# Kernel tuning notes

Hardware: AMD Instinct MI355X
Metric: run time of the kernel (lower is better)

## Reference

```python
import jax, jax.numpy as jnp
import numpy as np

N_NODES = 70839  # num_user + num_item from config
N_EDGES = 2_000_000
EMB_DIM = 64
EPS = 1e-12  # torch F.normalize default eps


def setup_inputs() -> dict:
    key = jax.random.key(0)
    k1, k2, k3, k4 = jax.random.split(key, 4)
    ego_embedding = jax.random.normal(k1, (N_NODES, EMB_DIM), dtype=jnp.float32)
    edge_weight = jax.random.uniform(k2, (N_EDGES,), dtype=jnp.float32)
    edge_src = jax.random.randint(k3, (N_EDGES,), 0, N_NODES, dtype=jnp.int32)
    edge_dst = jax.random.randint(k4, (N_EDGES,), 0, N_NODES, dtype=jnp.int32)
    return {
        "ego_embedding": ego_embedding,
        "edge_weight": edge_weight,
        "edge_src": edge_src,
        "edge_dst": edge_dst,
    }


def reference(ego_embedding, edge_weight, edge_src, edge_dst):
    # message: m_e = h[src_e] * w_e   (u_mul_e)
    m = ego_embedding[edge_src] * edge_weight[:, None]          # [E, D]
    # reduce: h_v = sum_{e: dst_e = v} m_e   (fn.sum)
    h = jax.ops.segment_sum(m, edge_dst, num_segments=N_NODES)  # [N, D]
    # F.normalize(h, dim=1, p=2): x / max(||x||_2, eps)
    norm = jnp.linalg.norm(h, axis=1, keepdims=True)
    return h / jnp.maximum(norm, EPS)
```

## Files before the change

kernel.cpp:

```cpp
#include <hip/hip_runtime.h>
#include <hip/hip_fp16.h>

#define EMB_D 64
#define SB 1024
#define SPAN 128
#define MAXG 1024
#define MAXK 3072
#define NCHUNK2 512
#define CHMAX 4096
#define TILE 4096
#define SLICE_SH 14
#define CAST_BLOCKS 256


__device__ __forceinline__ float h15_to_float(unsigned int bits) {
    return __half2float(__ushort_as_half((unsigned short)bits));
}

__global__ void a1_cast_histK(const float2* __restrict__ embin,
                              __half2* __restrict__ emb16, int n2,
                              const int* __restrict__ src,
                              const int* __restrict__ dst,
                              int* __restrict__ cntT,
                              int E, int NK, int S, int chunk) {
    if (blockIdx.x < CAST_BLOCKS) {
        int i = blockIdx.x * blockDim.x + threadIdx.x;
        int st = CAST_BLOCKS * blockDim.x;
        for (; i < n2; i += st)
            emb16[i] = __float22half2_rn(embin[i]);
    } else {
        __shared__ int bins[MAXK];
        int hb = blockIdx.x - CAST_BLOCKS;
        for (int k = threadIdx.x; k < NK; k += blockDim.x) bins[k] = 0;
        __syncthreads();
        int beg = hb * chunk;
        int end = min(beg + chunk, E);
        for (int i = beg + threadIdx.x; i < end; i += blockDim.x) {
            int key = (dst[i] >> 7) * S + (src[i] >> SLICE_SH);
            atomicAdd(&bins[key], 1);
        }
        __syncthreads();
        for (int k = threadIdx.x; k < NK; k += blockDim.x)
            cntT[k * NCHUNK2 + hb] = bins[k];
    }
}

__global__ void a1_cast_hist(const float2* __restrict__ embin,
                             __half2* __restrict__ emb16, int n2,
                             const int* __restrict__ dst,
                             int* __restrict__ cntT,
                             int E, int G, int chunk) {
    if (blockIdx.x < CAST_BLOCKS) {
        int i = blockIdx.x * blockDim.x + threadIdx.x;
        int st = CAST_BLOCKS * blockDim.x;
        for (; i < n2; i += st)
            emb16[i] = __float22half2_rn(embin[i]);
    } else {
        __shared__ int bins[MAXG];
        int hb = blockIdx.x - CAST_BLOCKS;
        for (int g = threadIdx.x; g < G; g += blockDim.x) bins[g] = 0;
        __syncthreads();
        int beg = hb * chunk;
        int end = min(beg + chunk, E);
        for (int i = beg + threadIdx.x; i < end; i += blockDim.x)
            atomicAdd(&bins[dst[i] >> 7], 1);
        __syncthreads();
        for (int g = threadIdx.x; g < G; g += blockDim.x)
            cntT[g * NCHUNK2 + hb] = bins[g];
    }
}

__global__ void scan_reduceB(const int* __restrict__ counts,
                             int* __restrict__ partial, int M) {
    __shared__ int wsum[16];
    const int tid = threadIdx.x, lane = tid & 63, wid = tid >> 6;
    int i = blockIdx.x * SB + tid;
    int v = (i < M) ? counts[i] : 0;
    #pragma unroll
    for (int off = 32; off > 0; off >>= 1)
        v += __shfl_xor(v, off, 64);
    if (lane == 0) wsum[wid] = v;
    __syncthreads();
    if (tid == 0) {
        int s = 0;
        #pragma unroll
        for (int k = 0; k < 16; ++k) s += wsum[k];
        partial[blockIdx.x] = s;
    }
}

__global__ void scan_partials(const int* __restrict__ partial,
                              int* __restrict__ blockoff,
                              int* __restrict__ offsets, int numB, int M) {
    __shared__ int wsum[16];
    __shared__ int wpre[16];
    __shared__ int carry;
    const int tid = threadIdx.x, lane = tid & 63, wid = tid >> 6;
    if (tid == 0) carry = 0;
    const int nPass = (numB + SB - 1) / SB;
    for (int p = 0; p < nPass; ++p) {
        __syncthreads();
        int base = carry;
        int idx = p * SB + tid;
        int v = (idx < numB) ? partial[idx] : 0;
        int x = v;
        #pragma unroll
        for (int off = 1; off < 64; off <<= 1) {
            int t = __shfl_up(x, off, 64);
            if (lane >= off) x += t;
        }
        if (lane == 63) wsum[wid] = x;
        __syncthreads();
        if (wid == 0) {
            int s = (lane < 16) ? wsum[lane] : 0;
            #pragma unroll
            for (int off = 1; off < 16; off <<= 1) {
                int t = __shfl_up(s, off, 64);
                if (lane >= off) s += t;
            }
            if (lane < 16) wpre[lane] = s;
        }
        __syncthreads();
        int excl = base + ((wid > 0) ? wpre[wid - 1] : 0) + (x - v);
        if (idx < numB) blockoff[idx] = excl;
        __syncthreads();
        if (tid == 0) carry = base + wpre[15];
    }
    __syncthreads();
    if (tid == 0) offsets[M] = carry;
}

__global__ void scan_applyB(const int* __restrict__ counts,
                            const int* __restrict__ blockoff,
                            int* __restrict__ offsets, int M) {
    __shared__ int wsum[16];
    __shared__ int wpre[16];
    const int tid = threadIdx.x, lane = tid & 63, wid = tid >> 6;
    int i = blockIdx.x * SB + tid;
    int v = (i < M) ? counts[i] : 0;
    int x = v;
    #pragma unroll
    for (int off = 1; off < 64; off <<= 1) {
        int t = __shfl_up(x, off, 64);
        if (lane >= off) x += t;
    }
    if (lane == 63) wsum[wid] = x;
    __syncthreads();
    if (wid == 0) {
        int s = (lane < 16) ? wsum[lane] : 0;
        #pragma unroll
        for (int off = 1; off < 16; off <<= 1) {
            int t = __shfl_up(s, off, 64);
            if (lane >= off) s += t;
        }
        if (lane < 16) wpre[lane] = s;
    }
    __syncthreads();
    int excl = blockoff[blockIdx.x] + ((wid > 0) ? wpre[wid - 1] : 0) + (x - v);
    if (i < M) offsets[i] = excl;
}

__global__ void scan_apply_ip(int* __restrict__ data,
                              const int* __restrict__ blockoff, int M) {
    __shared__ int wsum[16];
    __shared__ int wpre[16];
    const int tid = threadIdx.x, lane = tid & 63, wid = tid >> 6;
    int i = blockIdx.x * SB + tid;
    int v = (i < M) ? data[i] : 0;
    int x = v;
    #pragma unroll
    for (int off = 1; off < 64; off <<= 1) {
        int t = __shfl_up(x, off, 64);
        if (lane >= off) x += t;
    }
    if (lane == 63) wsum[wid] = x;
    __syncthreads();
    if (wid == 0) {
        int s = (lane < 16) ? wsum[lane] : 0;
        #pragma unroll
        for (int off = 1; off < 16; off <<= 1) {
            int t = __shfl_up(s, off, 64);
            if (lane >= off) s += t;
        }
        if (lane < 16) wpre[lane] = s;
    }
    __syncthreads();
    int excl = blockoff[blockIdx.x] + ((wid > 0) ? wpre[wid - 1] : 0) + (x - v);
    if (i < M) data[i] = excl;
}

__global__ __launch_bounds__(512) void partition_sortK(
        const int* __restrict__ src,
        const int* __restrict__ dst,
        const float* __restrict__ w,
        const int* __restrict__ scanT,
        uint2* __restrict__ stream8,
        int E, int NK, int S, int chunk) {
    __shared__ uint2 recs[CHMAX];
    __shared__ int cur[MAXK];
    __shared__ int delta[MAXK];
    __shared__ int wtot[8];

    const int tid = threadIdx.x, lane = tid & 63, wv = tid >> 6;
    const int b = blockIdx.x;
    const int beg = b * chunk;
    const int end = min(beg + chunk, E);
    const int n = end - beg;

    const int K = (NK + 511) >> 9;
    int vals[6], bases[6];
    int acc = 0;
    #pragma unroll
    for (int k = 0; k < 6; ++k) {
        int key = tid * K + k;
        int c = 0, bs = 0;
        if (k < K && key < NK) {
            bs = scanT[key * NCHUNK2 + b];
            c = scanT[key * NCHUNK2 + b + 1] - bs;
        }
        vals[k] = c;
        bases[k] = bs;
        acc += c;
    }
    int x = acc;
    #pragma unroll
    for (int off = 1; off < 64; off <<= 1) {
        int t = __shfl_up(x, off, 64);
        if (lane >= off) x += t;
    }
    if (lane == 63) wtot[wv] = x;
    __syncthreads();
    int woff = 0;
    #pragma unroll
    for (int k2 = 0; k2 < 8; ++k2)
        woff += (k2 < wv) ? wtot[k2] : 0;
    int run = woff + x - acc;
    #pragma unroll
    for (int k = 0; k < 6; ++k) {
        int key = tid * K + k;
        if (k < K && key < NK) {
            cur[key] = run;
            delta[key] = bases[k] - run;
            run += vals[k];
        }
    }
    __syncthreads();

    for (int i = beg + tid; i < end; i += 512) {
        int d = dst[i];
        int key = (d >> 7) * S + (src[i] >> SLICE_SH);
        unsigned int wb = __half_as_ushort(__float2half_rn(w[i]));
        unsigned int pk = ((unsigned int)src[i] << 15) | (wb & 0x7FFFu);
        int j = atomicAdd(&cur[key], 1);
        recs[j] = make_uint2(pk, (unsigned int)(d & (SPAN - 1)) |
                                 ((unsigned int)key << 7));
    }
    __syncthreads();

    for (int j = tid; j < n; j += 512) {
        uint2 r = recs[j];
        int key = (int)(r.y >> 7);
        stream8[delta[key] + j] = make_uint2(r.x, r.y & (SPAN - 1u));
    }
}

__global__ __launch_bounds__(512) void partition_sort(
        const int* __restrict__ src,
        const int* __restrict__ dst,
        const float* __restrict__ w,
        const int* __restrict__ cntT,
        const int* __restrict__ scanT,
        uint2* __restrict__ stream8,
        int E, int G, int chunk) {
    __shared__ uint2 recs[CHMAX];
    __shared__ int cur[MAXG];
    __shared__ int delta[MAXG];
    __shared__ int wtot[8];

    const int tid = threadIdx.x, lane = tid & 63, wv = tid >> 6;
    const int b = blockIdx.x;
    const int beg = b * chunk;
    const int end = min(beg + chunk, E);
    const int n = end - beg;

    const int K = (G + 511) >> 9;
    int vals[2];
    int acc = 0;
    #pragma unroll
    for (int k = 0; k < 2; ++k) {
        int g = tid * K + k;
        int c = (k < K && g < G) ? cntT[g * NCHUNK2 + b] : 0;
        vals[k] = c;
        acc += c;
    }
    int x = acc;
    #pragma unroll
    for (int off = 1; off < 64; off <<= 1) {
        int t = __shfl_up(x, off, 64);
        if (lane >= off) x += t;
    }
    if (lane == 63) wtot[wv] = x;
    __syncthreads();
    int woff = 0;
    #pragma unroll
    for (int k2 = 0; k2 < 8; ++k2)
        woff += (k2 < wv) ? wtot[k2] : 0;
    int run = woff + x - acc;
    #pragma unroll
    for (int k = 0; k < 2; ++k) {
        int g = tid * K + k;
        if (k < K && g < G) {
            cur[g] = run;
            delta[g] = scanT[g * NCHUNK2 + b] - run;
            run += vals[k];
        }
    }
    __syncthreads();

    for (int i = beg + tid; i < end; i += 512) {
        int d = dst[i];
        unsigned int wb = __half_as_ushort(__float2half_rn(w[i]));
        unsigned int pk = ((unsigned int)src[i] << 15) | (wb & 0x7FFFu);
        int g = d >> 7;
        int j = atomicAdd(&cur[g], 1);
        recs[j] = make_uint2(pk, (unsigned int)(d & (SPAN - 1)) |
                                 ((unsigned int)g << 7));
    }
    __syncthreads();

    for (int j = tid; j < n; j += 512) {
        uint2 r = recs[j];
        int g = (int)(r.y >> 7);
        stream8[delta[g] + j] = make_uint2(r.x, r.y & (SPAN - 1u));
    }
}

__global__ __launch_bounds__(512) void gather_fused(
        const char* __restrict__ emb16b,
        const uint2* __restrict__ stream8,
        const int* __restrict__ scanT,
        float* __restrict__ out, int N, int SN) {
    __shared__ uint2 lrec[TILE];
    __shared__ unsigned int srt[TILE];
    __shared__ int hcnt[SPAN];
    __shared__ int nstart[SPAN];
    __shared__ int cur[SPAN];
    __shared__ int wtot[2];

    const int g = blockIdx.x;
    const int tid = threadIdx.x;
    const int lane = tid & 63, wv = tid >> 6;
    const int base = scanT[(size_t)g * SN];
    const int endE = scanT[(size_t)(g + 1) * SN];
    const int crew = tid >> 4;
    const int ql = tid & 15;
    const int sub = ql >> 3;
    const int sl = ql & 7;
    const unsigned qlo = (unsigned)(sl << 4);

    float4 accA[4], accB[4];
    #pragma unroll
    for (int ni = 0; ni < 4; ++ni) {
        accA[ni] = make_float4(0.f, 0.f, 0.f, 0.f);
        accB[ni] = make_float4(0.f, 0.f, 0.f, 0.f);
    }

    for (int tb = base; tb < endE; tb += TILE) {
        const int n = min(TILE, endE - tb);
        if (tid < SPAN) hcnt[tid] = 0;
        __syncthreads();
        for (int j = tid; j < n; j += 512) {
            uint2 r = stream8[tb + j];
            lrec[j] = r;
            atomicAdd(&hcnt[r.y], 1);
        }
        __syncthreads();
        int v = (tid < SPAN) ? hcnt[tid] : 0;
        int x = v;
        #pragma unroll
        for (int off = 1; off < 64; off <<= 1) {
            int t = __shfl_up(x, off, 64);
            if (lane >= off) x += t;
        }
        if (wv < 2 && lane == 63) wtot[wv] = x;
        __syncthreads();
        if (tid < SPAN) {
            int excl = x - v + ((wv == 1) ? wtot[0] : 0);
            nstart[tid] = excl;
            cur[tid] = excl;
        }
        __syncthreads();
        for (int j = tid; j < n; j += 512) {
            uint2 r = lrec[j];
            int slot = atomicAdd(&cur[r.y], 1);
            srt[slot] = r.x;
        }
        __syncthreads();
        #pragma unroll
        for (int ni = 0; ni < 4; ++ni) {
            int nd = crew + (ni << 5);
            int s = nstart[nd];
            int e = cur[nd];
            float4 aA = accA[ni];
            float4 aB = accB[ni];
            int k0 = s + sub;
            unsigned int pk0 = (k0 < e) ? srt[k0] : 0u;
            uint4 r0 = *reinterpret_cast<const uint4*>(
                emb16b + ((pk0 >> 15) * 128u + qlo));
            for (int k = k0; k < e; k += 2) {
                int k1 = k + 2;
                unsigned int pk1 = (k1 < e) ? srt[k1] : 0u;
                uint4 r1 = *reinterpret_cast<const uint4*>(
                    emb16b + ((pk1 >> 15) * 128u + qlo));
                float wt = h15_to_float(pk0 & 0x7FFFu);
                float2 x01 = __half22float2(*reinterpret_cast<__half2*>(&r0.x));
                float2 x23 = __half22float2(*reinterpret_cast<__half2*>(&r0.y));
                float2 x45 = __half22float2(*reinterpret_cast<__half2*>(&r0.z));
                float2 x67 = __half22float2(*reinterpret_cast<__half2*>(&r0.w));
                aA.x = fmaf(x01.x, wt, aA.x);
                aA.y = fmaf(x01.y, wt, aA.y);
                aA.z = fmaf(x23.x, wt, aA.z);
                aA.w = fmaf(x23.y, wt, aA.w);
                aB.x = fmaf(x45.x, wt, aB.x);
                aB.y = fmaf(x45.y, wt, aB.y);
                aB.z = fmaf(x67.x, wt, aB.z);
                aB.w = fmaf(x67.y, wt, aB.w);
                pk0 = pk1; r0 = r1;
            }
            accA[ni] = aA;
            accB[ni] = aB;
        }
        __syncthreads();
    }

    #pragma unroll
    for (int ni = 0; ni < 4; ++ni) {
        accA[ni].x += __shfl_xor(accA[ni].x, 8, 64);
        accA[ni].y += __shfl_xor(accA[ni].y, 8, 64);
        accA[ni].z += __shfl_xor(accA[ni].z, 8, 64);
        accA[ni].w += __shfl_xor(accA[ni].w, 8, 64);
        accB[ni].x += __shfl_xor(accB[ni].x, 8, 64);
        accB[ni].y += __shfl_xor(accB[ni].y, 8, 64);
        accB[ni].z += __shfl_xor(accB[ni].z, 8, 64);
        accB[ni].w += __shfl_xor(accB[ni].w, 8, 64);
        int node = g * SPAN + crew + (ni << 5);
        float4 aA = accA[ni];
        float4 aB = accB[ni];
        float ss = aA.x * aA.x + aA.y * aA.y + aA.z * aA.z + aA.w * aA.w
                 + aB.x * aB.x + aB.y * aB.y + aB.z * aB.z + aB.w * aB.w;
        ss += __shfl_xor(ss, 1, 64);
        ss += __shfl_xor(ss, 2, 64);
        ss += __shfl_xor(ss, 4, 64);
        float scale = 1.0f / fmaxf(sqrtf(ss), 1e-12f);
        if (node < N) {
            float4 a = sub ? aB : aA;
            float4 o = make_float4(a.x * scale, a.y * scale,
                                   a.z * scale, a.w * scale);
            *reinterpret_cast<float4*>(out + (size_t)node * EMB_D
                                       + (sl << 3) + (sub << 2)) = o;
        }
    }
}

__global__ void lightgcn_scatter(const float* __restrict__ emb,
                                 const float* __restrict__ w,
                                 const int* __restrict__ src,
                                 const int* __restrict__ dst,
                                 float* __restrict__ h, int E) {
    long long t = (long long)blockIdx.x * blockDim.x + threadIdx.x;
    int e = (int)(t >> 4);
    int d = (int)(t & 15) << 2;
    if (e >= E) return;
    int s = src[e]; int v = dst[e]; float wt = w[e];
    const float4 m = *reinterpret_cast<const float4*>(emb + (size_t)s * EMB_D + d);
    float* o = h + (size_t)v * EMB_D + d;
    unsafeAtomicAdd(o + 0, m.x * wt);
    unsafeAtomicAdd(o + 1, m.y * wt);
    unsafeAtomicAdd(o + 2, m.z * wt);
    unsafeAtomicAdd(o + 3, m.w * wt);
}

__global__ void lightgcn_normalize(float* __restrict__ h, int N) {
    int row = blockIdx.x * (blockDim.x >> 6) + (threadIdx.x >> 6);
    int lane = threadIdx.x & 63;
    if (row >= N) return;
    float x = h[(size_t)row * EMB_D + lane];
    float ss = x * x;
    #pragma unroll
    for (int off = 32; off > 0; off >>= 1)
        ss += __shfl_xor(ss, off, 64);
    h[(size_t)row * EMB_D + lane] = x / fmaxf(sqrtf(ss), 1e-12f);
}

extern "C" void kernel_launch(void* const* d_in, const int* in_sizes, int n_in,
                              void* d_out, int out_size, void* d_ws, size_t ws_size,
                              hipStream_t stream) {
    const float* emb = (const float*)d_in[0];
    const float* w   = (const float*)d_in[1];
    const int*   src = (const int*)d_in[2];
    const int*   dst = (const int*)d_in[3];
    float* out = (float*)d_out;

    const int N = in_sizes[0] / EMB_D;
    const int E = in_sizes[1];
    const int block = 256;
    const int G = (N + SPAN - 1) / SPAN;

    const int S4 = (N + (1 << SLICE_SH) - 1) >> SLICE_SH;
    const int NK4 = G * S4;
    const int M4 = NK4 * NCHUNK2;
    const int numB4 = (M4 + SB - 1) / SB;
    const int chunk4 = (E + NCHUNK2 - 1) / NCHUNK2;
    const int SN4 = S4 * NCHUNK2;
    size_t intsA7 = (size_t)(M4 + 1) + 2 * (size_t)numB4;
    size_t strOff7 = (intsA7 * sizeof(int) + 15) & ~(size_t)15;
    size_t embOff7 = (strOff7 + (size_t)E * sizeof(uint2) + 15) & ~(size_t)15;
    size_t neededA7 = embOff7 + (size_t)N * EMB_D * sizeof(__half);

    const int M3 = G * NCHUNK2;
    const int numB3 = (M3 + SB - 1) / SB;
    const int chunk3 = (E + NCHUNK2 - 1) / NCHUNK2;
    size_t intsA5 = (size_t)M3 + (size_t)(M3 + 1) + 2 * (size_t)numB3;
    size_t strOff5 = (intsA5 * sizeof(int) + 15) & ~(size_t)15;
    size_t embOff5 = (strOff5 + (size_t)E * sizeof(uint2) + 15) & ~(size_t)15;
    size_t neededA5 = embOff5 + (size_t)N * EMB_D * sizeof(__half);

    if (ws_size >= neededA7 && NK4 <= MAXK && chunk4 <= CHMAX &&
        E < (1 << 28) && N < (1 << 17)) {
        int* cntT     = (int*)d_ws;
        int* partial  = cntT + M4 + 1;
        int* blockoff = partial + numB4;
        uint2* stream8 = (uint2*)((char*)d_ws + strOff7);
        __half2* emb16 = (__half2*)((char*)d_ws + embOff7);

        int n2 = N * (EMB_D / 2);

        a1_cast_histK<<<CAST_BLOCKS + NCHUNK2, block, 0, stream>>>(
            (const float2*)emb, emb16, n2, src, dst, cntT, E, NK4, S4, chunk4);

        scan_reduceB<<<numB4, SB, 0, stream>>>(cntT, partial, M4);
        scan_partials<<<1, SB, 0, stream>>>(partial, blockoff, cntT, numB4, M4);
        scan_apply_ip<<<numB4, SB, 0, stream>>>(cntT, blockoff, M4);

        partition_sortK<<<NCHUNK2, 512, 0, stream>>>(src, dst, w, cntT,
                                                     stream8, E, NK4, S4,
                                                     chunk4);
        gather_fused<<<G, 512, 0, stream>>>((const char*)emb16, stream8, cntT,
                                            out, N, SN4);
    } else if (ws_size >= neededA5 && G <= MAXG && chunk3 <= CHMAX &&
               E < (1 << 28) && N < (1 << 17)) {
        int* cntT     = (int*)d_ws;
        int* scanT    = cntT + M3;
        int* partial  = scanT + M3 + 1;
        int* blockoff = partial + numB3;
        uint2* stream8 = (uint2*)((char*)d_ws + strOff5);
        __half2* emb16 = (__half2*)((char*)d_ws + embOff5);

        int n2 = N * (EMB_D / 2);

        a1_cast_hist<<<CAST_BLOCKS + NCHUNK2, block, 0, stream>>>(
            (const float2*)emb, emb16, n2, dst, cntT, E, G, chunk3);

        scan_reduceB<<<numB3, SB, 0, stream>>>(cntT, partial, M3);
        scan_partials<<<1, SB, 0, stream>>>(partial, blockoff, scanT, numB3, M3);
        scan_applyB<<<numB3, SB, 0, stream>>>(cntT, blockoff, scanT, M3);

        partition_sort<<<NCHUNK2, 512, 0, stream>>>(src, dst, w, cntT, scanT,
                                                    stream8, E, G, chunk3);

        gather_fused<<<G, 512, 0, stream>>>((const char*)emb16, stream8,
                                            scanT, out, N, NCHUNK2);
    } else {
        hipMemsetAsync(d_out, 0, (size_t)out_size * sizeof(float), stream);
        long long total = (long long)E * 16;
        int grid = (int)((total + block - 1) / block);
        lightgcn_scatter<<<grid, block, 0, stream>>>(emb, w, src, dst, out, E);
        int gridN = (N + 3) / 4;
        lightgcn_normalize<<<gridN, 256, 0, stream>>>(out, N);
    }
}
```

Before: 205.2 us.

## Replace global src-slice keyed partition with in-block slice sort and soft grid barrier

Drops the partition path keyed on (dst group, src slice), which needed a much larger histogram and scan, and returns to the partition keyed only on dst group. Source-slice locality is now rebuilt inside the gather kernel: each block bins its edges by (src slice, dst) in shared memory and walks the slices in order. A spin-based soft grid barrier after each slice keeps all blocks reading the same region of the half-precision embedding table, aiming for better L2 reuse. The barrier gives up after a bounded number of spins, so it only loosely synchronises blocks and may add sleep latency. It also assumes all 554 blocks are resident at once.

```diff
diff --git a/kernel.cpp b/kernel.cpp
--- a/kernel.cpp
+++ b/kernel.cpp
@@ -5,44 +5,17 @@
 #define SB 1024
 #define SPAN 128
 #define MAXG 1024
-#define MAXK 3072
 #define NCHUNK2 512
 #define CHMAX 4096
 #define TILE 4096
 #define SLICE_SH 14
+#define MAXS 8
+#define SKEYBINS (MAXS * SPAN)
 #define CAST_BLOCKS 256
 
 
 __device__ __forceinline__ float h15_to_float(unsigned int bits) {
     return __half2float(__ushort_as_half((unsigned short)bits));
-}
-
-__global__ void a1_cast_histK(const float2* __restrict__ embin,
-                              __half2* __restrict__ emb16, int n2,
-                              const int* __restrict__ src,
-                              const int* __restrict__ dst,
-                              int* __restrict__ cntT,
-                              int E, int NK, int S, int chunk) {
-    if (blockIdx.x < CAST_BLOCKS) {
-        int i = blockIdx.x * blockDim.x + threadIdx.x;
-        int st = CAST_BLOCKS * blockDim.x;
-        for (; i < n2; i += st)
-            emb16[i] = __float22half2_rn(embin[i]);
-    } else {
-        __shared__ int bins[MAXK];
-        int hb = blockIdx.x - CAST_BLOCKS;
-        for (int k = threadIdx.x; k < NK; k += blockDim.x) bins[k] = 0;
-        __syncthreads();
-        int beg = hb * chunk;
-        int end = min(beg + chunk, E);
-        for (int i = beg + threadIdx.x; i < end; i += blockDim.x) {
-            int key = (dst[i] >> 7) * S + (src[i] >> SLICE_SH);
-            atomicAdd(&bins[key], 1);
-        }
-        __syncthreads();
-        for (int k = threadIdx.x; k < NK; k += blockDim.x)
-            cntT[k * NCHUNK2 + hb] = bins[k];
-    }
 }
 
 __global__ void a1_cast_hist(const float2* __restrict__ embin,
@@ -160,110 +133,6 @@
     if (i < M) offsets[i] = excl;
 }
 
-__global__ void scan_apply_ip(int* __restrict__ data,
-                              const int* __restrict__ blockoff, int M) {
-    __shared__ int wsum[16];
-    __shared__ int wpre[16];
-    const int tid = threadIdx.x, lane = tid & 63, wid = tid >> 6;
-    int i = blockIdx.x * SB + tid;
-    int v = (i < M) ? data[i] : 0;
-    int x = v;
-    #pragma unroll
-    for (int off = 1; off < 64; off <<= 1) {
-        int t = __shfl_up(x, off, 64);
-        if (lane >= off) x += t;
-    }
-    if (lane == 63) wsum[wid] = x;
-    __syncthreads();
-    if (wid == 0) {
-        int s = (lane < 16) ? wsum[lane] : 0;
-        #pragma unroll
-        for (int off = 1; off < 16; off <<= 1) {
-            int t = __shfl_up(s, off, 64);
-            if (lane >= off) s += t;
-        }
-        if (lane < 16) wpre[lane] = s;
-    }
-    __syncthreads();
-    int excl = blockoff[blockIdx.x] + ((wid > 0) ? wpre[wid - 1] : 0) + (x - v);
-    if (i < M) data[i] = excl;
-}
-
-__global__ __launch_bounds__(512) void partition_sortK(
-        const int* __restrict__ src,
-        const int* __restrict__ dst,
-        const float* __restrict__ w,
-        const int* __restrict__ scanT,
-        uint2* __restrict__ stream8,
-        int E, int NK, int S, int chunk) {
-    __shared__ uint2 recs[CHMAX];
-    __shared__ int cur[MAXK];
-    __shared__ int delta[MAXK];
-    __shared__ int wtot[8];
-
-    const int tid = threadIdx.x, lane = tid & 63, wv = tid >> 6;
-    const int b = blockIdx.x;
-    const int beg = b * chunk;
-    const int end = min(beg + chunk, E);
-    const int n = end - beg;
-
-    const int K = (NK + 511) >> 9;
-    int vals[6], bases[6];
-    int acc = 0;
-    #pragma unroll
-    for (int k = 0; k < 6; ++k) {
-        int key = tid * K + k;
-        int c = 0, bs = 0;
-        if (k < K && key < NK) {
-            bs = scanT[key * NCHUNK2 + b];
-            c = scanT[key * NCHUNK2 + b + 1] - bs;
-        }
-        vals[k] = c;
-        bases[k] = bs;
-        acc += c;
-    }
-    int x = acc;
-    #pragma unroll
-    for (int off = 1; off < 64; off <<= 1) {
-        int t = __shfl_up(x, off, 64);
-        if (lane >= off) x += t;
-    }
-    if (lane == 63) wtot[wv] = x;
-    __syncthreads();
-    int woff = 0;
-    #pragma unroll
-    for (int k2 = 0; k2 < 8; ++k2)
-        woff += (k2 < wv) ? wtot[k2] : 0;
-    int run = woff + x - acc;
-    #pragma unroll
-    for (int k = 0; k < 6; ++k) {
-        int key = tid * K + k;
-        if (k < K && key < NK) {
-            cur[key] = run;
-            delta[key] = bases[k] - run;
-            run += vals[k];
-        }
-    }
-    __syncthreads();
-
-    for (int i = beg + tid; i < end; i += 512) {
-        int d = dst[i];
-        int key = (d >> 7) * S + (src[i] >> SLICE_SH);
-        unsigned int wb = __half_as_ushort(__float2half_rn(w[i]));
-        unsigned int pk = ((unsigned int)src[i] << 15) | (wb & 0x7FFFu);
-        int j = atomicAdd(&cur[key], 1);
-        recs[j] = make_uint2(pk, (unsigned int)(d & (SPAN - 1)) |
-                                 ((unsigned int)key << 7));
-    }
-    __syncthreads();
-
-    for (int j = tid; j < n; j += 512) {
-        uint2 r = recs[j];
-        int key = (int)(r.y >> 7);
-        stream8[delta[key] + j] = make_uint2(r.x, r.y & (SPAN - 1u));
-    }
-}
-
 __global__ __launch_bounds__(512) void partition_sort(
         const int* __restrict__ src,
         const int* __restrict__ dst,
@@ -332,6 +201,215 @@
         uint2 r = recs[j];
         int g = (int)(r.y >> 7);
         stream8[delta[g] + j] = make_uint2(r.x, r.y & (SPAN - 1u));
+    }
+}
+
+__device__ __forceinline__ void bin_scan(int* hcnt, int* nstart, int* cur,
+                                         int* wtot, int NB) {
+    const int tid = threadIdx.x, lane = tid & 63, wv = tid >> 6;
+    int b0 = tid << 1, b1 = b0 + 1;
+    int v0 = (b0 < NB) ? hcnt[b0] : 0;
+    int v1 = (b1 < NB) ? hcnt[b1] : 0;
+    int p = v0 + v1;
+    int x = p;
+    #pragma unroll
+    for (int off = 1; off < 64; off <<= 1) {
+        int t = __shfl_up(x, off, 64);
+        if (lane >= off) x += t;
+    }
+    if (lane == 63) wtot[wv] = x;
+    __syncthreads();
+    int woff = 0;
+    #pragma unroll
+    for (int k = 0; k < 8; ++k) woff += (k < wv) ? wtot[k] : 0;
+    int excl = woff + x - p;
+    if (b0 < NB) { nstart[b0] = excl; cur[b0] = excl; }
+    if (b1 < NB) { nstart[b1] = excl + v0; cur[b1] = excl + v0; }
+    __syncthreads();
+}
+
+__device__ __forceinline__ void soft_grid_sync(int* bar, int phase, int nblk) {
+    __syncthreads();
+    if (threadIdx.x == 0) {
+        int want = nblk * (phase + 1);
+        int got = atomicAdd(bar, 1) + 1;
+        int spins = 0;
+        while (got < want && spins < 1000) {
+            __builtin_amdgcn_s_sleep(32);
+            got = __hip_atomic_load(bar, __ATOMIC_RELAXED,
+                                    __HIP_MEMORY_SCOPE_AGENT);
+            ++spins;
+        }
+    }
+    __syncthreads();
+}
+
+__global__ __launch_bounds__(512) void gather_sliced(
+        const char* __restrict__ emb16b,
+        const uint2* __restrict__ stream8,
+        const int* __restrict__ scanT,
+        float* __restrict__ out, int N, int S, int* bar) {
+    __shared__ unsigned int srt[TILE];
+    __shared__ int hcnt[SKEYBINS];
+    __shared__ int nstart[SKEYBINS];
+    __shared__ int cur[SKEYBINS];
+    __shared__ int wtot[8];
+
+    const int g = blockIdx.x;
+    const int tid = threadIdx.x;
+    const int base = scanT[g * NCHUNK2];
+    const int endE = scanT[(g + 1) * NCHUNK2];
+    const int n = endE - base;
+    const int crew = tid >> 4;
+    const int ql = tid & 15;
+    const int sub = ql >> 3;
+    const int sl = ql & 7;
+    const unsigned qlo = (unsigned)(sl << 4);
+    const int nblk = gridDim.x;
+
+    float4 accA[4], accB[4];
+    #pragma unroll
+    for (int ni = 0; ni < 4; ++ni) {
+        accA[ni] = make_float4(0.f, 0.f, 0.f, 0.f);
+        accB[ni] = make_float4(0.f, 0.f, 0.f, 0.f);
+    }
+
+    if (n <= TILE) {
+        const int NB = S * SPAN;
+        for (int k = tid; k < NB; k += 512) hcnt[k] = 0;
+        __syncthreads();
+        for (int j = tid; j < n; j += 512) {
+            uint2 r = stream8[base + j];
+            int skey = (int)((r.x >> 15) >> SLICE_SH);
+            atomicAdd(&hcnt[(skey << 7) + (int)r.y], 1);
+        }
+        __syncthreads();
+        bin_scan(hcnt, nstart, cur, wtot, NB);
+        for (int j = tid; j < n; j += 512) {
+            uint2 r = stream8[base + j];
+            int skey = (int)((r.x >> 15) >> SLICE_SH);
+            int slot = atomicAdd(&cur[(skey << 7) + (int)r.y], 1);
+            srt[slot] = r.x;
+        }
+        __syncthreads();
+
+        for (int s = 0; s < S; ++s) {
+            #pragma unroll
+            for (int ni = 0; ni < 4; ++ni) {
+                int bin = (s << 7) + crew + (ni << 5);
+                int sB = nstart[bin];
+                int e = cur[bin];
+                float4 aA = accA[ni];
+                float4 aB = accB[ni];
+                int k0 = sB + sub;
+                unsigned int pk0 = (k0 < e) ? srt[k0] : 0u;
+                uint4 r0 = *reinterpret_cast<const uint4*>(
+                    emb16b + ((pk0 >> 15) * 128u + qlo));
+                for (int k = k0; k < e; k += 2) {
+                    int k1 = k + 2;
+                    unsigned int pk1 = (k1 < e) ? srt[k1] : 0u;
+                    uint4 r1 = *reinterpret_cast<const uint4*>(
+                        emb16b + ((pk1 >> 15) * 128u + qlo));
+                    float wt = h15_to_float(pk0 & 0x7FFFu);
+                    float2 x01 = __half22float2(*reinterpret_cast<__half2*>(&r0.x));
+                    float2 x23 = __half22float2(*reinterpret_cast<__half2*>(&r0.y));
+                    float2 x45 = __half22float2(*reinterpret_cast<__half2*>(&r0.z));
+                    float2 x67 = __half22float2(*reinterpret_cast<__half2*>(&r0.w));
+                    aA.x = fmaf(x01.x, wt, aA.x);
+                    aA.y = fmaf(x01.y, wt, aA.y);
+                    aA.z = fmaf(x23.x, wt, aA.z);
+                    aA.w = fmaf(x23.y, wt, aA.w);
+                    aB.x = fmaf(x45.x, wt, aB.x);
+                    aB.y = fmaf(x45.y, wt, aB.y);
+                    aB.z = fmaf(x67.x, wt, aB.z);
+                    aB.w = fmaf(x67.y, wt, aB.w);
+                    pk0 = pk1; r0 = r1;
+                }
+                accA[ni] = aA;
+                accB[ni] = aB;
+            }
+            if (s < S - 1) soft_grid_sync(bar, s, nblk);
+        }
+    } else {
+        for (int tb = base; tb < endE; tb += TILE) {
+            const int nt = min(TILE, endE - tb);
+            if (tid < SPAN) hcnt[tid] = 0;
+            __syncthreads();
+            for (int j = tid; j < nt; j += 512)
+                atomicAdd(&hcnt[stream8[tb + j].y], 1);
+            __syncthreads();
+            bin_scan(hcnt, nstart, cur, wtot, SPAN);
+            for (int j = tid; j < nt; j += 512) {
+                uint2 r = stream8[tb + j];
+                int slot = atomicAdd(&cur[(int)r.y], 1);
+                srt[slot] = r.x;
+            }
+            __syncthreads();
+            #pragma unroll
+            for (int ni = 0; ni < 4; ++ni) {
+                int bin = crew + (ni << 5);
+                int sB = nstart[bin];
+                int e = cur[bin];
+                float4 aA = accA[ni];
+                float4 aB = accB[ni];
+                int k0 = sB + sub;
+                unsigned int pk0 = (k0 < e) ? srt[k0] : 0u;
+                uint4 r0 = *reinterpret_cast<const uint4*>(
+                    emb16b + ((pk0 >> 15) * 128u + qlo));
+                for (int k = k0; k < e; k += 2) {
+                    int k1 = k + 2;
+                    unsigned int pk1 = (k1 < e) ? srt[k1] : 0u;
+                    uint4 r1 = *reinterpret_cast<const uint4*>(
+                        emb16b + ((pk1 >> 15) * 128u + qlo));
+                    float wt = h15_to_float(pk0 & 0x7FFFu);
+                    float2 x01 = __half22float2(*reinterpret_cast<__half2*>(&r0.x));
+                    float2 x23 = __half22float2(*reinterpret_cast<__half2*>(&r0.y));
+                    float2 x45 = __half22float2(*reinterpret_cast<__half2*>(&r0.z));
+                    float2 x67 = __half22float2(*reinterpret_cast<__half2*>(&r0.w));
+                    aA.x = fmaf(x01.x, wt, aA.x);
+                    aA.y = fmaf(x01.y, wt, aA.y);
+                    aA.z = fmaf(x23.x, wt, aA.z);
+                    aA.w = fmaf(x23.y, wt, aA.w);
+                    aB.x = fmaf(x45.x, wt, aB.x);
+                    aB.y = fmaf(x45.y, wt, aB.y);
+                    aB.z = fmaf(x67.x, wt, aB.z);
+                    aB.w = fmaf(x67.y, wt, aB.w);
+                    pk0 = pk1; r0 = r1;
+                }
+                accA[ni] = aA;
+                accB[ni] = aB;
+            }
+            __syncthreads();
+        }
+        for (int s = 0; s < S - 1; ++s) soft_grid_sync(bar, s, nblk);
+    }
+
+    #pragma unroll
+    for (int ni = 0; ni < 4; ++ni) {
+        accA[ni].x += __shfl_xor(accA[ni].x, 8, 64);
+        accA[ni].y += __shfl_xor(accA[ni].y, 8, 64);
+        accA[ni].z += __shfl_xor(accA[ni].z, 8, 64);
+        accA[ni].w += __shfl_xor(accA[ni].w, 8, 64);
+        accB[ni].x += __shfl_xor(accB[ni].x, 8, 64);
+        accB[ni].y += __shfl_xor(accB[ni].y, 8, 64);
+        accB[ni].z += __shfl_xor(accB[ni].z, 8, 64);
+        accB[ni].w += __shfl_xor(accB[ni].w, 8, 64);
+        int node = g * SPAN + crew + (ni << 5);
+        float4 aA = accA[ni];
+        float4 aB = accB[ni];
+        float ss = aA.x * aA.x + aA.y * aA.y + aA.z * aA.z + aA.w * aA.w
+                 + aB.x * aB.x + aB.y * aB.y + aB.z * aB.z + aB.w * aB.w;
+        ss += __shfl_xor(ss, 1, 64);
+        ss += __shfl_xor(ss, 2, 64);
+        ss += __shfl_xor(ss, 4, 64);
+        float scale = 1.0f / fmaxf(sqrtf(ss), 1e-12f);
+        if (node < N) {
+            float4 a = sub ? aB : aA;
+            float4 o = make_float4(a.x * scale, a.y * scale,
+                                   a.z * scale, a.w * scale);
+            *reinterpret_cast<float4*>(out + (size_t)node * EMB_D
+                                       + (sl << 3) + (sub << 2)) = o;
+        }
     }
 }
 
@@ -505,58 +583,30 @@
     const int E = in_sizes[1];
     const int block = 256;
     const int G = (N + SPAN - 1) / SPAN;
-
-    const int S4 = (N + (1 << SLICE_SH) - 1) >> SLICE_SH;
-    const int NK4 = G * S4;
-    const int M4 = NK4 * NCHUNK2;
-    const int numB4 = (M4 + SB - 1) / SB;
-    const int chunk4 = (E + NCHUNK2 - 1) / NCHUNK2;
-    const int SN4 = S4 * NCHUNK2;
-    size_t intsA7 = (size_t)(M4 + 1) + 2 * (size_t)numB4;
-    size_t strOff7 = (intsA7 * sizeof(int) + 15) & ~(size_t)15;
-    size_t embOff7 = (strOff7 + (size_t)E * sizeof(uint2) + 15) & ~(size_t)15;
-    size_t neededA7 = embOff7 + (size_t)N * EMB_D * sizeof(__half);
+    const int S = (N + (1 << SLICE_SH) - 1) >> SLICE_SH;
 
     const int M3 = G * NCHUNK2;
     const int numB3 = (M3 + SB - 1) / SB;
     const int chunk3 = (E + NCHUNK2 - 1) / NCHUNK2;
-    size_t intsA5 = (size_t)M3 + (size_t)(M3 + 1) + 2 * (size_t)numB3;
-    size_t strOff5 = (intsA5 * sizeof(int) + 15) & ~(size_t)15;
-    size_t embOff5 = (strOff5 + (size_t)E * sizeof(uint2) + 15) & ~(size_t)15;
-    size_t neededA5 = embOff5 + (size_t)N * EMB_D * sizeof(__half);
-
-    if (ws_size >= neededA7 && NK4 <= MAXK && chunk4 <= CHMAX &&
+
+    size_t intsA = (size_t)M3 + (size_t)(M3 + 1) + 2 * (size_t)numB3 + 1;
+    size_t strOff = (intsA * sizeof(int) + 15) & ~(size_t)15;
+    size_t embOff = (strOff + (size_t)E * sizeof(uint2) + 15) & ~(size_t)15;
+    size_t needed = embOff + (size_t)N * EMB_D * sizeof(__half);
+
+    if (ws_size >= needed && G <= MAXG && chunk3 <= CHMAX &&
         E < (1 << 28) && N < (1 << 17)) {
-        int* cntT     = (int*)d_ws;
-        int* partial  = cntT + M4 + 1;
-        int* blockoff = partial + numB4;
-        uint2* stream8 = (uint2*)((char*)d_ws + strOff7);
-        __half2* emb16 = (__half2*)((char*)d_ws + embOff7);
-
-        int n2 = N * (EMB_D / 2);
-
-        a1_cast_histK<<<CAST_BLOCKS + NCHUNK2, block, 0, stream>>>(
-            (const float2*)emb, emb16, n2, src, dst, cntT, E, NK4, S4, chunk4);
-
-        scan_reduceB<<<numB4, SB, 0, stream>>>(cntT, partial, M4);
-        scan_partials<<<1, SB, 0, stream>>>(partial, blockoff, cntT, numB4, M4);
-        scan_apply_ip<<<numB4, SB, 0, stream>>>(cntT, blockoff, M4);
-
-        partition_sortK<<<NCHUNK2, 512, 0, stream>>>(src, dst, w, cntT,
-                                                     stream8, E, NK4, S4,
-                                                     chunk4);
-        gather_fused<<<G, 512, 0, stream>>>((const char*)emb16, stream8, cntT,
-                                            out, N, SN4);
-    } else if (ws_size >= neededA5 && G <= MAXG && chunk3 <= CHMAX &&
-               E < (1 << 28) && N < (1 << 17)) {
         int* cntT     = (int*)d_ws;
         int* scanT    = cntT + M3;
         int* partial  = scanT + M3 + 1;
         int* blockoff = partial + numB3;
-        uint2* stream8 = (uint2*)((char*)d_ws + strOff5);
-        __half2* emb16 = (__half2*)((char*)d_ws + embOff5);
+        int* bar      = blockoff + numB3;
+        uint2* stream8 = (uint2*)((char*)d_ws + strOff);
+        __half2* emb16 = (__half2*)((char*)d_ws + embOff);
 
         int n2 = N * (EMB_D / 2);
+
+        hipMemsetAsync(bar, 0, sizeof(int), stream);
 
         a1_cast_hist<<<CAST_BLOCKS + NCHUNK2, block, 0, stream>>>(
             (const float2*)emb, emb16, n2, dst, cntT, E, G, chunk3);
@@ -568,8 +618,13 @@
         partition_sort<<<NCHUNK2, 512, 0, stream>>>(src, dst, w, cntT, scanT,
                                                     stream8, E, G, chunk3);
 
-        gather_fused<<<G, 512, 0, stream>>>((const char*)emb16, stream8,
-                                            scanT, out, N, NCHUNK2);
+        if (S <= MAXS) {
+            gather_sliced<<<G, 512, 0, stream>>>((const char*)emb16, stream8,
+                                                 scanT, out, N, S, bar);
+        } else {
+            gather_fused<<<G, 512, 0, stream>>>((const char*)emb16, stream8,
+                                                scanT, out, N, NCHUNK2);
+        }
     } else {
         hipMemsetAsync(d_out, 0, (size_t)out_size * sizeof(float), stream);
         long long total = (long long)E * 16;
```

Result: slower. 247.0 us (+20.4%).
